# Optimization experiments

Hardware: AMD Instinct MI355X
Metric: run time of the kernel (lower is better)

## Reference

```python
import jax, jax.numpy as jnp
import numpy as np


def setup_inputs() -> dict:
    key = jax.random.key(0)
    ks = jax.random.split(key, 6)
    B, T, D, H, O = 512, 1024, 64, 256, 64
    x_seq = jax.random.normal(ks[0], (B, T, D), dtype=jnp.float32)
    Wf = jax.random.normal(ks[1], (H, D + H), dtype=jnp.float32) * (1.0 / np.sqrt(D + H))
    bf = jax.random.normal(ks[2], (H,), dtype=jnp.float32) * 0.01
    tau = jnp.ones((H,), dtype=jnp.float32)
    A = jnp.ones((H,), dtype=jnp.float32)
    Wo = jax.random.normal(ks[3], (O, H), dtype=jnp.float32) * (1.0 / np.sqrt(H))
    bo = jax.random.normal(ks[4], (O,), dtype=jnp.float32) * 0.01
    return {"x_seq": x_seq, "Wf": Wf, "bf": bf, "tau": tau, "A": A, "Wo": Wo, "bo": bo}


def reference(x_seq, Wf, bf, tau, A, Wo, bo):
    # Liquid-time-constant RNN: h_{t+1} = h + (-(1/exp(tau) + f)*h + f*A)*dt
    # with f = sigmoid(Linear([x_t, h]))
    dt = jnp.float32(0.1)
    inv_tau = 1.0 / jnp.exp(tau)  # [H]
    B = x_seq.shape[0]
    H = tau.shape[0]
    h0 = jnp.zeros((B, H), dtype=x_seq.dtype)
    xs = jnp.swapaxes(x_seq, 0, 1)  # [T, B, D] for scan over time

    def step(h, x):
        inp = jnp.concatenate([x, h], axis=1)  # [B, D+H]
        f = jax.nn.sigmoid(inp @ Wf.T + bf)    # [B, H]
        dh = (-(inv_tau + f) * h + f * A) * dt
        return h + dh, None

    h_final, _ = jax.lax.scan(step, h0, xs)
    return h_final @ Wo.T + bo  # [B, O]
```

## Files before the change

kernel.cpp:

```cpp
#include <hip/hip_runtime.h>
#include <hip/hip_bf16.h>


typedef __attribute__((ext_vector_type(8))) short bf16x8;
typedef __attribute__((ext_vector_type(4))) float f32x4;
typedef __attribute__((ext_vector_type(2))) float f32x2;

#define T_STEPS 1024
#define D_IN    64
#define H_DIM   256
#define O_DIM   64
#define ROWS    16
#define NTHREADS 512
#define LDS_STRIDE 640

__device__ __forceinline__ short f2bf(float x) {
    union { float f; unsigned u; } v; v.f = x;
    unsigned r = (v.u + 0x7FFFu + ((v.u >> 16) & 1u)) >> 16;
    return (short)r;
}
__device__ __forceinline__ unsigned pack2(float a, float b) {
    return ((unsigned)(unsigned short)f2bf(b) << 16) | (unsigned)(unsigned short)f2bf(a);
}
__device__ __forceinline__ float sigm(float z) {
    float e = __builtin_amdgcn_exp2f(-1.4426950408889634f * z);
    return __builtin_amdgcn_rcpf(1.0f + e);
}

__global__ __launch_bounds__(NTHREADS, 2)
void ltc_kernel(const float* __restrict__ x_seq,
                const float* __restrict__ Wf,
                const float* __restrict__ bf_,
                const float* __restrict__ tau,
                const float* __restrict__ Avec,
                const float* __restrict__ Wo,
                const float* __restrict__ bo,
                float* __restrict__ out)
{
    __shared__ alignas(64) char lds_raw[ROWS * LDS_STRIDE];

    const int tid  = threadIdx.x;
    const int lane = tid & 63;
    const int w    = tid >> 6;
    const int lcol = lane & 15;
    const int lgrp = lane >> 4;
    const int brow0 = blockIdx.x * ROWS;
    const int jbase = w * 32;

    bf16x8 bfrag[10][2];
    #pragma unroll
    for (int nt = 0; nt < 2; ++nt) {
        const int j = jbase + nt * 16 + lcol;
        const float* wrow = Wf + j * (D_IN + H_DIM);
        #pragma unroll
        for (int kt = 0; kt < 10; ++kt) {
            const int k0 = kt * 32 + lgrp * 8;
            f32x4 w0 = *(const f32x4*)(wrow + k0);
            f32x4 w1 = *(const f32x4*)(wrow + k0 + 4);
            bf16x8 b;
            b[0] = f2bf(w0[0]); b[1] = f2bf(w0[1]); b[2] = f2bf(w0[2]); b[3] = f2bf(w0[3]);
            b[4] = f2bf(w1[0]); b[5] = f2bf(w1[1]); b[6] = f2bf(w1[2]); b[7] = f2bf(w1[3]);
            bfrag[kt][nt] = b;
        }
    }

    const float dt = 0.1f;
    float bias[2], ctau[2], cA[2];
    #pragma unroll
    for (int nt = 0; nt < 2; ++nt) {
        const int j = jbase + nt * 16 + lcol;
        bias[nt] = bf_[j];
        ctau[nt] = 1.0f - dt * __builtin_amdgcn_rcpf(__expf(tau[j]));
        cA[nt]   = dt * Avec[j];
    }

    for (int i = tid; i < (ROWS * LDS_STRIDE) / 4; i += NTHREADS)
        ((unsigned*)lds_raw)[i] = 0u;
    __syncthreads();

    const int xrow = tid >> 5;
    const int xpos = tid & 31;
    const float* xbase = x_seq + ((size_t)(brow0 + xrow) * T_STEPS) * D_IN + xpos * 2;
    const int xbyte = xrow * LDS_STRIDE + ((xpos * 4) ^ ((xrow & 7) << 4));
    {
        f32x2 x0 = *(const f32x2*)(xbase);
        *(unsigned*)(lds_raw + xbyte) = pack2(x0[0], x0[1]);
    }
    __syncthreads();

    const int arow = lcol;
    const char* abase = lds_raw + arow * LDS_STRIDE;
    const int aswz = (arow & 7) << 4;

    float h0[4] = {0.f, 0.f, 0.f, 0.f};
    float h1[4] = {0.f, 0.f, 0.f, 0.f};

    for (int t = 0; t < T_STEPS; ++t) {
        const int tn = (t + 1 < T_STEPS) ? (t + 1) : (T_STEPS - 1);
        f32x2 xv = *(const f32x2*)(xbase + (size_t)tn * D_IN);

        bf16x8 afrag[10];
        #pragma unroll
        for (int kt = 0; kt < 10; ++kt) {
            const int off = (kt * 64 + lgrp * 16) ^ aswz;
            afrag[kt] = *(const bf16x8*)(abase + off);
        }

        f32x4 acc0 = { bias[0], bias[0], bias[0], bias[0] };
        f32x4 acc1 = { bias[1], bias[1], bias[1], bias[1] };
        #pragma unroll
        for (int kt = 0; kt < 10; ++kt) {
            acc0 = __builtin_amdgcn_mfma_f32_16x16x32_bf16(afrag[kt], bfrag[kt][0], acc0, 0, 0, 0);
            acc1 = __builtin_amdgcn_mfma_f32_16x16x32_bf16(afrag[kt], bfrag[kt][1], acc1, 0, 0, 0);
        }

        short hb0[4], hb1[4];
        #pragma unroll
        for (int r = 0; r < 4; ++r) {
            float f0 = sigm(acc0[r]);
            h0[r] = h0[r] * (ctau[0] - dt * f0) + cA[0] * f0;
            hb0[r] = f2bf(h0[r]);
            float f1 = sigm(acc1[r]);
            h1[r] = h1[r] * (ctau[1] - dt * f1) + cA[1] * f1;
            hb1[r] = f2bf(h1[r]);
        }

        __syncthreads();

        #pragma unroll
        for (int r = 0; r < 4; ++r) {
            const int m = lgrp * 4 + r;
            const int msw = (m & 7) << 4;
            const int kb0 = 2 * D_IN + 2 * (jbase + 0 * 16 + lcol);
            const int kb1 = 2 * D_IN + 2 * (jbase + 1 * 16 + lcol);
            *(short*)(lds_raw + m * LDS_STRIDE + (kb0 ^ msw)) = hb0[r];
            *(short*)(lds_raw + m * LDS_STRIDE + (kb1 ^ msw)) = hb1[r];
        }
        *(unsigned*)(lds_raw + xbyte) = pack2(xv[0], xv[1]);

        __syncthreads();
    }

    if (w < 4) {
        bf16x8 ha[8];
        #pragma unroll
        for (int kt = 0; kt < 8; ++kt) {
            const int off = (2 * D_IN + kt * 64 + lgrp * 16) ^ aswz;
            ha[kt] = *(const bf16x8*)(abase + off);
        }
        const int o = w * 16 + lcol;
        const float* worow = Wo + o * H_DIM;
        const float bov = bo[o];
        f32x4 acc = { bov, bov, bov, bov };
        #pragma unroll
        for (int kt = 0; kt < 8; ++kt) {
            const int k0 = kt * 32 + lgrp * 8;
            f32x4 w0 = *(const f32x4*)(worow + k0);
            f32x4 w1 = *(const f32x4*)(worow + k0 + 4);
            bf16x8 b;
            b[0] = f2bf(w0[0]); b[1] = f2bf(w0[1]); b[2] = f2bf(w0[2]); b[3] = f2bf(w0[3]);
            b[4] = f2bf(w1[0]); b[5] = f2bf(w1[1]); b[6] = f2bf(w1[2]); b[7] = f2bf(w1[3]);
            acc = __builtin_amdgcn_mfma_f32_16x16x32_bf16(ha[kt], b, acc, 0, 0, 0);
        }
        #pragma unroll
        for (int r = 0; r < 4; ++r) {
            const int m = lgrp * 4 + r;
            out[(size_t)(brow0 + m) * O_DIM + o] = acc[r];
        }
    }
}

extern "C" void kernel_launch(void* const* d_in, const int* in_sizes, int n_in,
                              void* d_out, int out_size, void* d_ws, size_t ws_size,
                              hipStream_t stream) {
    const float* x_seq = (const float*)d_in[0];
    const float* Wf    = (const float*)d_in[1];
    const float* bf_   = (const float*)d_in[2];
    const float* tau   = (const float*)d_in[3];
    const float* Avec  = (const float*)d_in[4];
    const float* Wo    = (const float*)d_in[5];
    const float* bo    = (const float*)d_in[6];
    float* out = (float*)d_out;

    ltc_kernel<<<512 / ROWS, NTHREADS, 0, stream>>>(x_seq, Wf, bf_, tau, Avec, Wo, bo, out);
}
```

Baseline: 1.042 ms.

## Double-buffer LDS state and halve block size to drop one barrier per step

Switches to a ping-pong LDS buffer so each timestep reads the previous buffer and writes the next, removing one of the two block barriers per step. The block shrinks from 8 to 4 waves, each computing 64 hidden columns (four MFMA accumulators), and x loads widen to four floats per thread. This cuts synchronization on the serial recurrence but doubles per-wave MFMA work and register pressure and halves wave-level parallelism per block. After 1024 steps the final state sits in buffer 0, which the epilogue reads.

```diff
diff --git a/kernel.cpp b/kernel.cpp
--- a/kernel.cpp
+++ b/kernel.cpp
@@ -3,31 +3,28 @@
 
 
 typedef __attribute__((ext_vector_type(8))) short bf16x8;
+typedef __attribute__((ext_vector_type(4))) short short4v;
 typedef __attribute__((ext_vector_type(4))) float f32x4;
-typedef __attribute__((ext_vector_type(2))) float f32x2;
 
 #define T_STEPS 1024
 #define D_IN    64
 #define H_DIM   256
 #define O_DIM   64
 #define ROWS    16
-#define NTHREADS 512
+#define NTHREADS 256
 #define LDS_STRIDE 640
+#define BUFSZ   (ROWS * LDS_STRIDE)
 
 __device__ __forceinline__ short f2bf(float x) {
-    union { float f; unsigned u; } v; v.f = x;
-    unsigned r = (v.u + 0x7FFFu + ((v.u >> 16) & 1u)) >> 16;
-    return (short)r;
-}
-__device__ __forceinline__ unsigned pack2(float a, float b) {
-    return ((unsigned)(unsigned short)f2bf(b) << 16) | (unsigned)(unsigned short)f2bf(a);
+    __hip_bfloat16 b = __float2bfloat16(x);
+    return *reinterpret_cast<short*>(&b);
 }
 __device__ __forceinline__ float sigm(float z) {
     float e = __builtin_amdgcn_exp2f(-1.4426950408889634f * z);
     return __builtin_amdgcn_rcpf(1.0f + e);
 }
 
-__global__ __launch_bounds__(NTHREADS, 2)
+__global__ __launch_bounds__(NTHREADS, 1)
 void ltc_kernel(const float* __restrict__ x_seq,
                 const float* __restrict__ Wf,
                 const float* __restrict__ bf_,
@@ -37,7 +34,7 @@
                 const float* __restrict__ bo,
                 float* __restrict__ out)
 {
-    __shared__ alignas(64) char lds_raw[ROWS * LDS_STRIDE];
+    __shared__ alignas(64) char lds_raw[2 * BUFSZ];
 
     const int tid  = threadIdx.x;
     const int lane = tid & 63;
@@ -45,11 +42,11 @@
     const int lcol = lane & 15;
     const int lgrp = lane >> 4;
     const int brow0 = blockIdx.x * ROWS;
-    const int jbase = w * 32;
+    const int jbase = w * 64;
 
-    bf16x8 bfrag[10][2];
+    bf16x8 bfrag[10][4];
     #pragma unroll
-    for (int nt = 0; nt < 2; ++nt) {
+    for (int nt = 0; nt < 4; ++nt) {
         const int j = jbase + nt * 16 + lcol;
         const float* wrow = Wf + j * (D_IN + H_DIM);
         #pragma unroll
@@ -65,88 +62,102 @@
     }
 
     const float dt = 0.1f;
-    float bias[2], ctau[2], cA[2];
+    float bias[4], ctau[4], cA[4];
     #pragma unroll
-    for (int nt = 0; nt < 2; ++nt) {
+    for (int nt = 0; nt < 4; ++nt) {
         const int j = jbase + nt * 16 + lcol;
         bias[nt] = bf_[j];
         ctau[nt] = 1.0f - dt * __builtin_amdgcn_rcpf(__expf(tau[j]));
         cA[nt]   = dt * Avec[j];
     }
 
-    for (int i = tid; i < (ROWS * LDS_STRIDE) / 4; i += NTHREADS)
+    for (int i = tid; i < (2 * BUFSZ) / 4; i += NTHREADS)
         ((unsigned*)lds_raw)[i] = 0u;
     __syncthreads();
 
-    const int xrow = tid >> 5;
-    const int xpos = tid & 31;
-    const float* xbase = x_seq + ((size_t)(brow0 + xrow) * T_STEPS) * D_IN + xpos * 2;
-    const int xbyte = xrow * LDS_STRIDE + ((xpos * 4) ^ ((xrow & 7) << 4));
+    const int xrow = tid >> 4;
+    const int xpos = tid & 15;
+    const float* xbase = x_seq + ((size_t)(brow0 + xrow) * T_STEPS) * D_IN + xpos * 4;
+    const int xbyte = xrow * LDS_STRIDE + ((xpos * 8) ^ ((xrow & 7) << 4));
     {
-        f32x2 x0 = *(const f32x2*)(xbase);
-        *(unsigned*)(lds_raw + xbyte) = pack2(x0[0], x0[1]);
+        f32x4 x0 = *(const f32x4*)(xbase);
+        short4v xs = { f2bf(x0[0]), f2bf(x0[1]), f2bf(x0[2]), f2bf(x0[3]) };
+        *(short4v*)(lds_raw + xbyte) = xs;
     }
     __syncthreads();
 
     const int arow = lcol;
-    const char* abase = lds_raw + arow * LDS_STRIDE;
+    const int abase_off = arow * LDS_STRIDE;
     const int aswz = (arow & 7) << 4;
 
-    float h0[4] = {0.f, 0.f, 0.f, 0.f};
-    float h1[4] = {0.f, 0.f, 0.f, 0.f};
+    int kbyte[4];
+    #pragma unroll
+    for (int nt = 0; nt < 4; ++nt) kbyte[nt] = 2 * D_IN + 2 * (jbase + nt * 16 + lcol);
 
+    float h[4][4] = {};
+
+    int p = 0;
     for (int t = 0; t < T_STEPS; ++t) {
+        const char* rbuf = lds_raw + p * BUFSZ;
+        char*       wbuf = lds_raw + (p ^ 1) * BUFSZ;
+
         const int tn = (t + 1 < T_STEPS) ? (t + 1) : (T_STEPS - 1);
-        f32x2 xv = *(const f32x2*)(xbase + (size_t)tn * D_IN);
+        f32x4 xv = *(const f32x4*)(xbase + (size_t)tn * D_IN);
 
         bf16x8 afrag[10];
         #pragma unroll
         for (int kt = 0; kt < 10; ++kt) {
             const int off = (kt * 64 + lgrp * 16) ^ aswz;
-            afrag[kt] = *(const bf16x8*)(abase + off);
+            afrag[kt] = *(const bf16x8*)(rbuf + abase_off + off);
         }
 
-        f32x4 acc0 = { bias[0], bias[0], bias[0], bias[0] };
-        f32x4 acc1 = { bias[1], bias[1], bias[1], bias[1] };
+        f32x4 acc[4];
+        #pragma unroll
+        for (int nt = 0; nt < 4; ++nt)
+            acc[nt] = f32x4{ bias[nt], bias[nt], bias[nt], bias[nt] };
         #pragma unroll
         for (int kt = 0; kt < 10; ++kt) {
-            acc0 = __builtin_amdgcn_mfma_f32_16x16x32_bf16(afrag[kt], bfrag[kt][0], acc0, 0, 0, 0);
-            acc1 = __builtin_amdgcn_mfma_f32_16x16x32_bf16(afrag[kt], bfrag[kt][1], acc1, 0, 0, 0);
+            #pragma unroll
+            for (int nt = 0; nt < 4; ++nt)
+                acc[nt] = __builtin_amdgcn_mfma_f32_16x16x32_bf16(afrag[kt], bfrag[kt][nt], acc[nt], 0, 0, 0);
         }
 
-        short hb0[4], hb1[4];
+        short hb[4][4];
         #pragma unroll
-        for (int r = 0; r < 4; ++r) {
-            float f0 = sigm(acc0[r]);
-            h0[r] = h0[r] * (ctau[0] - dt * f0) + cA[0] * f0;
-            hb0[r] = f2bf(h0[r]);
-            float f1 = sigm(acc1[r]);
-            h1[r] = h1[r] * (ctau[1] - dt * f1) + cA[1] * f1;
-            hb1[r] = f2bf(h1[r]);
+        for (int nt = 0; nt < 4; ++nt) {
+            #pragma unroll
+            for (int r = 0; r < 4; ++r) {
+                float f = sigm(acc[nt][r]);
+                h[nt][r] = h[nt][r] * (ctau[nt] - dt * f) + cA[nt] * f;
+                hb[nt][r] = f2bf(h[nt][r]);
+            }
         }
-
-        __syncthreads();
 
         #pragma unroll
         for (int r = 0; r < 4; ++r) {
             const int m = lgrp * 4 + r;
+            const int mrow = m * LDS_STRIDE;
             const int msw = (m & 7) << 4;
-            const int kb0 = 2 * D_IN + 2 * (jbase + 0 * 16 + lcol);
-            const int kb1 = 2 * D_IN + 2 * (jbase + 1 * 16 + lcol);
-            *(short*)(lds_raw + m * LDS_STRIDE + (kb0 ^ msw)) = hb0[r];
-            *(short*)(lds_raw + m * LDS_STRIDE + (kb1 ^ msw)) = hb1[r];
+            #pragma unroll
+            for (int nt = 0; nt < 4; ++nt)
+                *(short*)(wbuf + mrow + (kbyte[nt] ^ msw)) = hb[nt][r];
         }
-        *(unsigned*)(lds_raw + xbyte) = pack2(xv[0], xv[1]);
+        {
+            short4v xs = { f2bf(xv[0]), f2bf(xv[1]), f2bf(xv[2]), f2bf(xv[3]) };
+            *(short4v*)(wbuf + xbyte) = xs;
+        }
 
         __syncthreads();
+        p ^= 1;
     }
 
-    if (w < 4) {
+    {
+        const char* fbuf = lds_raw;
         bf16x8 ha[8];
         #pragma unroll
         for (int kt = 0; kt < 8; ++kt) {
             const int off = (2 * D_IN + kt * 64 + lgrp * 16) ^ aswz;
-            ha[kt] = *(const bf16x8*)(abase + off);
+            ha[kt] = *(const bf16x8*)(fbuf + abase_off + off);
         }
         const int o = w * 16 + lcol;
         const float* worow = Wo + o * H_DIM;
```

Measured after the change: 1.602 ms. +53.7%, slower.

## Double-buffer hidden state in LDS and feed x fragments from registers

Applied to the files above, without the earlier changes.

The single LDS buffer is replaced with two ping-pong buffers that hold only the hidden state, which removes one of the two barriers per time step. Each lane now loads its x slice straight from global memory into registers as an MFMA A-fragment and prefetches the next step's slice. Hidden columns are interleaved so each lane writes two adjacent bf16 values with one 32-bit store. The update is also reassociated to shorten the dependent chain after the sigmoid. The cost is more LDS, a changed hidden-column mapping, and per-lane 16-byte global loads of x every step.

```diff
diff --git a/kernel.cpp b/kernel.cpp
--- a/kernel.cpp
+++ b/kernel.cpp
@@ -4,7 +4,6 @@
 
 typedef __attribute__((ext_vector_type(8))) short bf16x8;
 typedef __attribute__((ext_vector_type(4))) float f32x4;
-typedef __attribute__((ext_vector_type(2))) float f32x2;
 
 #define T_STEPS 1024
 #define D_IN    64
@@ -12,19 +11,22 @@
 #define O_DIM   64
 #define ROWS    16
 #define NTHREADS 512
-#define LDS_STRIDE 640
+#define HSTRIDE 512
+#define BUFSZ   (ROWS * HSTRIDE)
 
 __device__ __forceinline__ short f2bf(float x) {
-    union { float f; unsigned u; } v; v.f = x;
-    unsigned r = (v.u + 0x7FFFu + ((v.u >> 16) & 1u)) >> 16;
-    return (short)r;
-}
-__device__ __forceinline__ unsigned pack2(float a, float b) {
-    return ((unsigned)(unsigned short)f2bf(b) << 16) | (unsigned)(unsigned short)f2bf(a);
+    __hip_bfloat16 b = __float2bfloat16(x);
+    return *reinterpret_cast<short*>(&b);
 }
 __device__ __forceinline__ float sigm(float z) {
     float e = __builtin_amdgcn_exp2f(-1.4426950408889634f * z);
     return __builtin_amdgcn_rcpf(1.0f + e);
+}
+__device__ __forceinline__ bf16x8 pack8(f32x4 a, f32x4 b) {
+    bf16x8 r;
+    r[0]=f2bf(a[0]); r[1]=f2bf(a[1]); r[2]=f2bf(a[2]); r[3]=f2bf(a[3]);
+    r[4]=f2bf(b[0]); r[5]=f2bf(b[1]); r[6]=f2bf(b[2]); r[7]=f2bf(b[3]);
+    return r;
 }
 
 __global__ __launch_bounds__(NTHREADS, 2)
@@ -37,7 +39,7 @@
                 const float* __restrict__ bo,
                 float* __restrict__ out)
 {
-    __shared__ alignas(64) char lds_raw[ROWS * LDS_STRIDE];
+    __shared__ alignas(64) char lds_raw[2 * BUFSZ];
 
     const int tid  = threadIdx.x;
     const int lane = tid & 63;
@@ -45,22 +47,21 @@
     const int lcol = lane & 15;
     const int lgrp = lane >> 4;
     const int brow0 = blockIdx.x * ROWS;
-    const int jbase = w * 32;
+    const int j0 = w * 32 + 2 * lcol;
 
-    bf16x8 bfrag[10][2];
+    bf16x8 bh[8][2], bx[2][2];
     #pragma unroll
     for (int nt = 0; nt < 2; ++nt) {
-        const int j = jbase + nt * 16 + lcol;
-        const float* wrow = Wf + j * (D_IN + H_DIM);
+        const float* wrow = Wf + (j0 + nt) * (D_IN + H_DIM);
         #pragma unroll
-        for (int kt = 0; kt < 10; ++kt) {
-            const int k0 = kt * 32 + lgrp * 8;
-            f32x4 w0 = *(const f32x4*)(wrow + k0);
-            f32x4 w1 = *(const f32x4*)(wrow + k0 + 4);
-            bf16x8 b;
-            b[0] = f2bf(w0[0]); b[1] = f2bf(w0[1]); b[2] = f2bf(w0[2]); b[3] = f2bf(w0[3]);
-            b[4] = f2bf(w1[0]); b[5] = f2bf(w1[1]); b[6] = f2bf(w1[2]); b[7] = f2bf(w1[3]);
-            bfrag[kt][nt] = b;
+        for (int kt = 0; kt < 8; ++kt) {
+            const int k0 = D_IN + kt * 32 + lgrp * 8;
+            bh[kt][nt] = pack8(*(const f32x4*)(wrow + k0), *(const f32x4*)(wrow + k0 + 4));
+        }
+        #pragma unroll
+        for (int kx = 0; kx < 2; ++kx) {
+            const int k0 = kx * 32 + lgrp * 8;
+            bx[kx][nt] = pack8(*(const f32x4*)(wrow + k0), *(const f32x4*)(wrow + k0 + 4));
         }
     }
 
@@ -68,86 +69,99 @@
     float bias[2], ctau[2], cA[2];
     #pragma unroll
     for (int nt = 0; nt < 2; ++nt) {
-        const int j = jbase + nt * 16 + lcol;
+        const int j = j0 + nt;
         bias[nt] = bf_[j];
         ctau[nt] = 1.0f - dt * __builtin_amdgcn_rcpf(__expf(tau[j]));
         cA[nt]   = dt * Avec[j];
     }
 
-    for (int i = tid; i < (ROWS * LDS_STRIDE) / 4; i += NTHREADS)
+    for (int i = tid; i < (2 * BUFSZ) / 4; i += NTHREADS)
         ((unsigned*)lds_raw)[i] = 0u;
+
+    const float* xrow = x_seq + (size_t)(brow0 + lcol) * T_STEPS * D_IN + lgrp * 8;
+    f32x4 nx0 = *(const f32x4*)(xrow);
+    f32x4 nx1 = *(const f32x4*)(xrow + 4);
+    f32x4 nx2 = *(const f32x4*)(xrow + 32);
+    f32x4 nx3 = *(const f32x4*)(xrow + 36);
+
     __syncthreads();
 
-    const int xrow = tid >> 5;
-    const int xpos = tid & 31;
-    const float* xbase = x_seq + ((size_t)(brow0 + xrow) * T_STEPS) * D_IN + xpos * 2;
-    const int xbyte = xrow * LDS_STRIDE + ((xpos * 4) ^ ((xrow & 7) << 4));
-    {
-        f32x2 x0 = *(const f32x2*)(xbase);
-        *(unsigned*)(lds_raw + xbyte) = pack2(x0[0], x0[1]);
+    bf16x8 xc0 = pack8(nx0, nx1);
+    bf16x8 xc1 = pack8(nx2, nx3);
+
+    const int aswz  = (lcol & 7) << 4;
+    const int rbase = lcol * HSTRIDE;
+    int roff[8];
+    #pragma unroll
+    for (int kt = 0; kt < 8; ++kt)
+        roff[kt] = rbase + ((kt * 64 + lgrp * 16) ^ aswz);
+    int woff[4];
+    #pragma unroll
+    for (int r = 0; r < 4; ++r) {
+        const int m = lgrp * 4 + r;
+        woff[r] = m * HSTRIDE + ((2 * j0) ^ ((m & 7) << 4));
     }
-    __syncthreads();
-
-    const int arow = lcol;
-    const char* abase = lds_raw + arow * LDS_STRIDE;
-    const int aswz = (arow & 7) << 4;
 
     float h0[4] = {0.f, 0.f, 0.f, 0.f};
     float h1[4] = {0.f, 0.f, 0.f, 0.f};
 
     for (int t = 0; t < T_STEPS; ++t) {
-        const int tn = (t + 1 < T_STEPS) ? (t + 1) : (T_STEPS - 1);
-        f32x2 xv = *(const f32x2*)(xbase + (size_t)tn * D_IN);
+        const char* rbuf = lds_raw + (t & 1) * BUFSZ;
+        char*       wbuf = lds_raw + ((t & 1) ^ 1) * BUFSZ;
 
-        bf16x8 afrag[10];
+        bf16x8 ah[8];
         #pragma unroll
-        for (int kt = 0; kt < 10; ++kt) {
-            const int off = (kt * 64 + lgrp * 16) ^ aswz;
-            afrag[kt] = *(const bf16x8*)(abase + off);
+        for (int kt = 0; kt < 8; ++kt)
+            ah[kt] = *(const bf16x8*)(rbuf + roff[kt]);
+
+        const int tn = (t + 1 < T_STEPS) ? (t + 1) : t;
+        const float* xp = xrow + (size_t)tn * D_IN;
+        nx0 = *(const f32x4*)(xp);
+        nx1 = *(const f32x4*)(xp + 4);
+        nx2 = *(const f32x4*)(xp + 32);
+        nx3 = *(const f32x4*)(xp + 36);
+
+        f32x4 a0 = { bias[0], bias[0], bias[0], bias[0] };
+        f32x4 a1 = { bias[1], bias[1], bias[1], bias[1] };
+        a0 = __builtin_amdgcn_mfma_f32_16x16x32_bf16(xc0, bx[0][0], a0, 0, 0, 0);
+        a1 = __builtin_amdgcn_mfma_f32_16x16x32_bf16(xc0, bx[0][1], a1, 0, 0, 0);
+        a0 = __builtin_amdgcn_mfma_f32_16x16x32_bf16(xc1, bx[1][0], a0, 0, 0, 0);
+        a1 = __builtin_amdgcn_mfma_f32_16x16x32_bf16(xc1, bx[1][1], a1, 0, 0, 0);
+        #pragma unroll
+        for (int kt = 0; kt < 8; ++kt) {
+            a0 = __builtin_amdgcn_mfma_f32_16x16x32_bf16(ah[kt], bh[kt][0], a0, 0, 0, 0);
+            a1 = __builtin_amdgcn_mfma_f32_16x16x32_bf16(ah[kt], bh[kt][1], a1, 0, 0, 0);
         }
 
-        f32x4 acc0 = { bias[0], bias[0], bias[0], bias[0] };
-        f32x4 acc1 = { bias[1], bias[1], bias[1], bias[1] };
+        unsigned hw[4];
         #pragma unroll
-        for (int kt = 0; kt < 10; ++kt) {
-            acc0 = __builtin_amdgcn_mfma_f32_16x16x32_bf16(afrag[kt], bfrag[kt][0], acc0, 0, 0, 0);
-            acc1 = __builtin_amdgcn_mfma_f32_16x16x32_bf16(afrag[kt], bfrag[kt][1], acc1, 0, 0, 0);
+        for (int r = 0; r < 4; ++r) {
+            float f0 = sigm(a0[r]);
+            float u0 = cA[0] - dt * h0[r];
+            h0[r] = h0[r] * ctau[0] + f0 * u0;
+            float f1 = sigm(a1[r]);
+            float u1 = cA[1] - dt * h1[r];
+            h1[r] = h1[r] * ctau[1] + f1 * u1;
+            hw[r] = ((unsigned)(unsigned short)f2bf(h1[r]) << 16)
+                  |  (unsigned)(unsigned short)f2bf(h0[r]);
         }
 
-        short hb0[4], hb1[4];
-        #pragma unroll
-        for (int r = 0; r < 4; ++r) {
-            float f0 = sigm(acc0[r]);
-            h0[r] = h0[r] * (ctau[0] - dt * f0) + cA[0] * f0;
-            hb0[r] = f2bf(h0[r]);
-            float f1 = sigm(acc1[r]);
-            h1[r] = h1[r] * (ctau[1] - dt * f1) + cA[1] * f1;
-            hb1[r] = f2bf(h1[r]);
-        }
-
-        __syncthreads();
+        xc0 = pack8(nx0, nx1);
+        xc1 = pack8(nx2, nx3);
 
         #pragma unroll
-        for (int r = 0; r < 4; ++r) {
-            const int m = lgrp * 4 + r;
-            const int msw = (m & 7) << 4;
-            const int kb0 = 2 * D_IN + 2 * (jbase + 0 * 16 + lcol);
-            const int kb1 = 2 * D_IN + 2 * (jbase + 1 * 16 + lcol);
-            *(short*)(lds_raw + m * LDS_STRIDE + (kb0 ^ msw)) = hb0[r];
-            *(short*)(lds_raw + m * LDS_STRIDE + (kb1 ^ msw)) = hb1[r];
-        }
-        *(unsigned*)(lds_raw + xbyte) = pack2(xv[0], xv[1]);
+        for (int r = 0; r < 4; ++r)
+            *(unsigned*)(wbuf + woff[r]) = hw[r];
 
         __syncthreads();
     }
 
     if (w < 4) {
+        const char* fbuf = lds_raw;
         bf16x8 ha[8];
         #pragma unroll
-        for (int kt = 0; kt < 8; ++kt) {
-            const int off = (2 * D_IN + kt * 64 + lgrp * 16) ^ aswz;
-            ha[kt] = *(const bf16x8*)(abase + off);
-        }
+        for (int kt = 0; kt < 8; ++kt)
+            ha[kt] = *(const bf16x8*)(fbuf + roff[kt]);
         const int o = w * 16 + lcol;
         const float* worow = Wo + o * H_DIM;
         const float bov = bo[o];
@@ -155,12 +169,9 @@
         #pragma unroll
         for (int kt = 0; kt < 8; ++kt) {
             const int k0 = kt * 32 + lgrp * 8;
-            f32x4 w0 = *(const f32x4*)(worow + k0);
-            f32x4 w1 = *(const f32x4*)(worow + k0 + 4);
-            bf16x8 b;
-            b[0] = f2bf(w0[0]); b[1] = f2bf(w0[1]); b[2] = f2bf(w0[2]); b[3] = f2bf(w0[3]);
-            b[4] = f2bf(w1[0]); b[5] = f2bf(w1[1]); b[6] = f2bf(w1[2]); b[7] = f2bf(w1[3]);
-            acc = __builtin_amdgcn_mfma_f32_16x16x32_bf16(ha[kt], b, acc, 0, 0, 0);
+            acc = __builtin_amdgcn_mfma_f32_16x16x32_bf16(
+                ha[kt], pack8(*(const f32x4*)(worow + k0), *(const f32x4*)(worow + k0 + 4)),
+                acc, 0, 0, 0);
         }
         #pragma unroll
         for (int r = 0; r < 4; ++r) {
```

Measured after the change: 1.776 ms. 1.7x slower.
